# Kernel tuning notes

Measured on AMD Instinct MI355X. Metric: run time of the kernel, lower is better.

## Reference

```python
import jax, jax.numpy as jnp
import numpy as np

ITERS = 2
EPS = 1e-6

_OFFSETS = [(a, b, c) for a in (-1, 0, 1) for b in (-1, 0, 1) for c in (-1, 0, 1)]


def _erosion_step(im):
    # product over full 3x3x3 neighborhood (connectivity=26 -> all 27 voxels),
    # out-of-bounds padded with 1 (identity for product)
    B, C, D, H, W = im.shape
    p = jnp.pad(im, ((0, 0), (0, 0), (1, 1), (1, 1), (1, 1)), constant_values=1.0)
    prod = jnp.ones_like(im)
    for dz, dy, dx in _OFFSETS:
        prod = prod * p[:, :, 1 + dz:1 + dz + D, 1 + dy:1 + dy + H, 1 + dx:1 + dx + W]
    return prod


def _distance_map(im, iters=ITERS):
    # PositiveDistanceMap: dils = -SoftErosion3D(1-im) where SoftErosion3D
    # returns temp = -sum_k im_k (im_0 = 1-im, im_{k+1} = im_k * erosion(im_k))
    cur = 1.0 - im
    acc = jnp.zeros_like(cur)
    for _ in range(iters):
        acc = acc + cur
        cur = cur * _erosion_step(cur)
    return acc


def _lah_loss(x, y_onehot):
    axes = (2, 3, 4)  # batch_lah=False -> per (batch, class) reduction
    dm_hat = _distance_map(x)
    dm_gt = _distance_map(y_onehot)
    fp = (dm_gt * x).sum(axes)
    fn = (dm_hat * y_onehot).sum(axes)
    # norm == 0
    fp = fp / (x.sum(axes) + EPS)
    fn = fn / (y_onehot.sum(axes) + EPS)
    lah = (fp + fn + jnp.abs(fp - fn)) / 2  # logsum2 == elementwise max
    return lah[:, 1:].mean()  # do_bg=False drops background channel


def setup_inputs() -> dict:
    key = jax.random.key(0)
    k1, k2 = jax.random.split(key)
    x = jax.random.uniform(k1, (2, 4, 128, 128, 128), dtype=jnp.float32)
    y = jax.random.randint(k2, (2, 1, 128, 128, 128), 0, 4, dtype=jnp.int64)
    return {"x": x, "y": y}


def reference(x, y):
    C = x.shape[1]
    y_onehot = jax.nn.one_hot(y[:, 0], C, axis=1, dtype=x.dtype)  # [B,C,D,H,W]
    return _lah_loss(x, y_onehot)
```

## Files before the change

### kernel.cpp

```cpp
#include <hip/hip_runtime.h>

constexpr int SPB = 1 << 21;
constexpr float EPSV = 1e-6f;

__device__ unsigned char g_mask[2 * SPB];

constexpr int K0_ZSEG = 4;
constexpr int K0_NBLK = (2 * (128 / K0_ZSEG) * 128) / 4;

struct MEnt { int pk, cx, cy; };

__device__ __forceinline__ MEnt k0_load(const int* __restrict__ yb, int s,
                                        int rbase0, bool ym1, bool yp1) {
    MEnt e;
    const int rb = (s << 14) | rbase0;
    int2 vc = *(const int2*)(yb + rb);
    int nib0 = 1 << vc.x, nib1 = 1 << vc.y;
    if (ym1) { int2 vm = *(const int2*)(yb + rb - 128); nib0 |= 1 << vm.x; nib1 |= 1 << vm.y; }
    if (yp1) { int2 vp = *(const int2*)(yb + rb + 128); nib0 |= 1 << vp.x; nib1 |= 1 << vp.y; }
    e.pk = nib0 | (nib1 << 8);
    e.cx = vc.x; e.cy = vc.y;
    return e;
}

__global__ __launch_bounds__(256) void mask_build(const int* __restrict__ y32) {
    const int wid = (blockIdx.x << 2) | (threadIdx.x >> 6);
    const int lane = threadIdx.x & 63;
    const int yy = wid & 127;
    const int zs = (wid >> 7) & 31;
    const int b = (wid >> 12) & 1;
    const int x0 = lane << 1;
    const int z0 = zs * K0_ZSEG;
    const bool ym1 = yy > 0, yp1 = yy < 127;
    const int rbase0 = (yy << 7) | x0;

    const int* __restrict__ yb = y32 + ((long)b << 21);
    unsigned char* __restrict__ mb = g_mask + ((long)b << 21);

    MEnt e0, e1;
    if (z0 > 0) e0 = k0_load(yb, z0 - 1, rbase0, ym1, yp1);
    else { e0.pk = 0; e0.cx = 0; e0.cy = 0; }
    e1 = k0_load(yb, z0, rbase0, ym1, yp1);

#pragma unroll
    for (int dz = 0; dz < K0_ZSEG; ++dz) {
        const int z = z0 + dz;
        MEnt e2;
        if (z + 1 < 128) e2 = k0_load(yb, z + 1, rbase0, ym1, yp1);
        else { e2.pk = 0; e2.cx = 0; e2.cy = 0; }

        const int zor = e0.pk | e1.pk | e2.pk;
        int orL = __shfl_up(zor, 1);
        if (lane == 0) orL = 0;
        int orR = __shfl_down(zor, 1);
        if (lane == 63) orR = 0;
        const int full0 = (zor | (zor >> 8) | (orL >> 8)) & 15;
        const int full1 = (zor | (zor >> 8) | orR) & 15;

        const unsigned short st =
            (unsigned short)((full0 | (e1.cx << 4)) | ((full1 | (e1.cy << 4)) << 8));
        *(unsigned short*)(mb + ((z << 14) | rbase0)) = st;

        e0 = e1; e1 = e2;
    }
}

constexpr int ZC = 8;
constexpr int NBLK = 8 * 16 * (128 / ZC);

__global__ __launch_bounds__(256) void lah_main(const float* __restrict__ x,
                                                float* __restrict__ acc) {
    __shared__ float raw[4][10][128];
    __shared__ float sred[4];

    const int bid = blockIdx.x;
    const int plane = bid & 7;
    const int b = plane >> 2, cls = plane & 3;
    const int inner = bid >> 3;
    const int yc = inner & 15;
    const int zq = inner >> 4;
    const int r0 = yc * 8;
    const int z0 = zq * ZC;
    const int t = threadIdx.x;
    const int rr = t >> 5;
    const int xc = (t & 31) << 2;
    const int lane = t & 63;
    const int xrow = 8 + (t >> 5);

    const float* __restrict__ xp = x + ((long)plane << 21);
    const unsigned char* __restrict__ mb = g_mask + ((long)b << 21);
    const int mrow = (r0 + rr) << 7;

    const float4 Z4 = make_float4(0.f, 0.f, 0.f, 0.f);

    auto gload = [&](int k, int i) -> float4 {
        const int gr = r0 - 1 + i;
        if ((unsigned)k > 127u || (unsigned)gr > 127u)
            return make_float4(0.f, 0.f, 0.f, 0.f);
        return *(const float4*)(xp + ((k << 14) | (gr << 7) | xc));
    };
    auto stage_direct = [&](int k) {
        const int s = k & 3;
        *(float4*)&raw[s][rr][xc] = gload(k, rr);
        if (t < 64) *(float4*)&raw[s][xrow][xc] = gload(k, xrow);
    };
    auto yprod = [&](int s, float4& cx) -> float4 {
        const float4 a = *(const float4*)&raw[s][rr][xc];
        const float4 bq = *(const float4*)&raw[s][rr + 1][xc];
        const float4 c = *(const float4*)&raw[s][rr + 2][xc];
        cx = bq;
        float4 o;
        o.x = (1.f - a.x) * (1.f - bq.x) * (1.f - c.x);
        o.y = (1.f - a.y) * (1.f - bq.y) * (1.f - c.y);
        o.z = (1.f - a.z) * (1.f - bq.z) * (1.f - c.z);
        o.w = (1.f - a.w) * (1.f - bq.w) * (1.f - c.w);
        return o;
    };

    stage_direct(z0 - 1);
    stage_direct(z0);
    stage_direct(z0 + 1);
    float4 pA = gload(z0 + 2, rr);
    float4 pB = (t < 64) ? gload(z0 + 2, xrow) : Z4;
    __syncthreads();
    float4 cxd, cx0;
    float4 ypm1 = yprod((z0 - 1) & 3, cxd);
    float4 yp0 = yprod(z0 & 3, cx0);
    unsigned mcur = *(const unsigned*)(mb + ((z0 << 14) | mrow | xc));

    float fp = 0.f, fn = 0.f, sx = 0.f, sy = 0.f;

#pragma unroll
    for (int dz = 0; dz < ZC; ++dz) {
        const int z = z0 + dz;

        float4 nA = Z4, nB = Z4;
        if (dz <= ZC - 3) {
            nA = gload(z + 3, rr);
            if (t < 64) nB = gload(z + 3, xrow);
        }
        unsigned mnext = 0;
        if (dz <= ZC - 2)
            mnext = *(const unsigned*)(mb + (((z + 1) << 14) | mrow | xc));

        float4 cx1;
        const float4 ypp1 = yprod((z + 1) & 3, cx1);

        {
            const float zp0 = ypm1.x * yp0.x * ypp1.x;
            const float zp1 = ypm1.y * yp0.y * ypp1.y;
            const float zp2 = ypm1.z * yp0.z * ypp1.z;
            const float zp3 = ypm1.w * yp0.w * ypp1.w;
            float zl = __shfl_up(zp3, 1);
            if ((t & 31) == 0) zl = 1.f;
            float zr = __shfl_down(zp0, 1);
            if ((t & 31) == 31) zr = 1.f;
            const float t01 = zp0 * zp1, t12 = zp1 * zp2, t23 = zp2 * zp3;
            const float P[4] = {zl * t01, t01 * zp2, t12 * zp3, t23 * zr};
            const float xa[4] = {cx0.x, cx0.y, cx0.z, cx0.w};
#pragma unroll
            for (int j = 0; j < 4; ++j) {
                const int m = (mcur >> (j * 8)) & 0xFF;
                const bool pres = (m >> cls) & 1;
                const bool eq = (m >> 4) == cls;
                const float xv = xa[j];
                sx += xv;
                fp += eq ? 0.f : xv * (pres ? 1.f : 2.f);
                fn += eq ? (1.f - xv) * (1.f + P[j]) : 0.f;
                sy += eq ? 1.f : 0.f;
            }
        }

        if (dz <= ZC - 2) {
            const int s = (z + 2) & 3;
            *(float4*)&raw[s][rr][xc] = pA;
            if (t < 64) *(float4*)&raw[s][xrow][xc] = pB;
        }
        __syncthreads();

        pA = nA; pB = nB;
        ypm1 = yp0; yp0 = ypp1; cx0 = cx1; mcur = mnext;
    }

    float rr4[4] = {fp, fn, sx, sy};
#pragma unroll
    for (int i = 0; i < 4; ++i) {
        float vv = rr4[i];
#pragma unroll
        for (int off = 32; off >= 1; off >>= 1) vv += __shfl_down(vv, off);
        rr4[i] = vv;
    }
    if (t < 4) sred[t] = 0.f;
    __syncthreads();
    if (lane == 0) {
#pragma unroll
        for (int i = 0; i < 4; ++i) atomicAdd(&sred[i], rr4[i]);
    }
    __syncthreads();
    if (t < 4)
        atomicAdd(&acc[b * 16 + t * 4 + cls], sred[t]);
}

__global__ void lah_finalize(const float* __restrict__ acc, float* __restrict__ out) {
    float loss = 0.f;
#pragma unroll
    for (int b = 0; b < 2; ++b) {
#pragma unroll
        for (int c = 1; c < 4; ++c) {
            const float fp = acc[b * 16 + 0 + c];
            const float fn = acc[b * 16 + 4 + c];
            const float sxv = acc[b * 16 + 8 + c];
            const float syv = acc[b * 16 + 12 + c];
            loss += fmaxf(fp / (sxv + EPSV), fn / (syv + EPSV));
        }
    }
    out[0] = loss / 6.f;
}

extern "C" void kernel_launch(void* const* d_in, const int* in_sizes, int n_in,
                              void* d_out, int out_size, void* d_ws, size_t ws_size,
                              hipStream_t stream) {
    const float* x = (const float*)d_in[0];
    const int* y32 = (const int*)d_in[1];
    float* out = (float*)d_out;
    float* acc = (float*)d_ws;

    hipMemsetAsync(d_ws, 0, 32 * sizeof(float), stream);
    mask_build<<<K0_NBLK, 256, 0, stream>>>(y32);
    lah_main<<<NBLK, 256, 0, stream>>>(x, acc);
    lah_finalize<<<1, 1, 0, stream>>>(acc, out);
}
```

Baseline: 49.22 us.

## Give each wavefront a private LDS ring to drop per-slice block barriers

Each 64-lane wavefront now owns a two-output-row tile and stages its own four y-rows per z-slice into a wave-private LDS ring. Since no other wave reads that data, the per-iteration __syncthreads is removed, and loads are prefetched two slices ahead. The cost is more halo traffic: each wave loads 4 rows to produce 2, where before 10 rows were loaded to produce 8. It also depends on lockstep execution within a wavefront for the LDS ordering, and the loop unroll changes from full to 4.

```diff
diff --git a/kernel.cpp b/kernel.cpp
--- a/kernel.cpp
+++ b/kernel.cpp
@@ -70,44 +70,56 @@
 
 __global__ __launch_bounds__(256) void lah_main(const float* __restrict__ x,
                                                 float* __restrict__ acc) {
-    __shared__ float raw[4][10][128];
+    __shared__ float lds[4][4][4][128];
     __shared__ float sred[4];
 
     const int bid = blockIdx.x;
     const int plane = bid & 7;
     const int b = plane >> 2, cls = plane & 3;
     const int inner = bid >> 3;
-    const int yc = inner & 15;
+    const int quad = inner & 15;
     const int zq = inner >> 4;
-    const int r0 = yc * 8;
+    const int t = threadIdx.x;
+    const int w = t >> 6;
+    const int rp = quad * 4 + w;
+    const int lane = t & 63;
+    const int half = lane >> 5;
+    const int lx = lane & 31;
+    const int xc = lx << 2;
     const int z0 = zq * ZC;
-    const int t = threadIdx.x;
-    const int rr = t >> 5;
-    const int xc = (t & 31) << 2;
-    const int lane = t & 63;
-    const int xrow = 8 + (t >> 5);
+
+    const int rowA = 2 * rp - 1 + half;
+    const int rowB = 2 * rp + 1 + half;
+    const int rout = 2 * rp + half;
+    const bool okA = rowA >= 0;
+    const bool okB = rowB <= 127;
 
     const float* __restrict__ xp = x + ((long)plane << 21);
     const unsigned char* __restrict__ mb = g_mask + ((long)b << 21);
-    const int mrow = (r0 + rr) << 7;
 
     const float4 Z4 = make_float4(0.f, 0.f, 0.f, 0.f);
 
-    auto gload = [&](int k, int i) -> float4 {
-        const int gr = r0 - 1 + i;
-        if ((unsigned)k > 127u || (unsigned)gr > 127u)
-            return make_float4(0.f, 0.f, 0.f, 0.f);
-        return *(const float4*)(xp + ((k << 14) | (gr << 7) | xc));
-    };
-    auto stage_direct = [&](int k) {
+    auto gloadA = [&](int k) -> float4 {
+        if ((unsigned)k > 127u || !okA) return Z4;
+        return *(const float4*)(xp + ((k << 14) | (rowA << 7) | xc));
+    };
+    auto gloadB = [&](int k) -> float4 {
+        if ((unsigned)k > 127u || !okB) return Z4;
+        return *(const float4*)(xp + ((k << 14) | (rowB << 7) | xc));
+    };
+    auto lmask = [&](int k) -> unsigned {
+        return *(const unsigned*)(mb + ((k << 14) | (rout << 7) | xc));
+    };
+    auto wslice = [&](int k, float4 a, float4 bb) {
         const int s = k & 3;
-        *(float4*)&raw[s][rr][xc] = gload(k, rr);
-        if (t < 64) *(float4*)&raw[s][xrow][xc] = gload(k, xrow);
-    };
-    auto yprod = [&](int s, float4& cx) -> float4 {
-        const float4 a = *(const float4*)&raw[s][rr][xc];
-        const float4 bq = *(const float4*)&raw[s][rr + 1][xc];
-        const float4 c = *(const float4*)&raw[s][rr + 2][xc];
+        *(float4*)&lds[w][s][half][xc] = a;
+        *(float4*)&lds[w][s][2 + half][xc] = bb;
+    };
+    auto yprod = [&](int k, float4& cx) -> float4 {
+        const int s = k & 3;
+        const float4 a = *(const float4*)&lds[w][s][half][xc];
+        const float4 bq = *(const float4*)&lds[w][s][half + 1][xc];
+        const float4 c = *(const float4*)&lds[w][s][half + 2][xc];
         cx = bq;
         float4 o;
         o.x = (1.f - a.x) * (1.f - bq.x) * (1.f - c.x);
@@ -117,34 +129,34 @@
         return o;
     };
 
-    stage_direct(z0 - 1);
-    stage_direct(z0);
-    stage_direct(z0 + 1);
-    float4 pA = gload(z0 + 2, rr);
-    float4 pB = (t < 64) ? gload(z0 + 2, xrow) : Z4;
-    __syncthreads();
+    {
+        float4 a0 = gloadA(z0 - 1), b0 = gloadB(z0 - 1);
+        float4 a1 = gloadA(z0),     b1 = gloadB(z0);
+        wslice(z0 - 1, a0, b0);
+        wslice(z0, a1, b1);
+    }
+    float4 p0A = gloadA(z0 + 1), p0B = gloadB(z0 + 1);
+    float4 p1A = gloadA(z0 + 2), p1B = gloadB(z0 + 2);
+    unsigned mcur = lmask(z0);
     float4 cxd, cx0;
-    float4 ypm1 = yprod((z0 - 1) & 3, cxd);
-    float4 yp0 = yprod(z0 & 3, cx0);
-    unsigned mcur = *(const unsigned*)(mb + ((z0 << 14) | mrow | xc));
+    float4 ypm1 = yprod(z0 - 1, cxd);
+    float4 yp0 = yprod(z0, cx0);
 
     float fp = 0.f, fn = 0.f, sx = 0.f, sy = 0.f;
 
-#pragma unroll
+#pragma unroll 4
     for (int dz = 0; dz < ZC; ++dz) {
         const int z = z0 + dz;
 
         float4 nA = Z4, nB = Z4;
-        if (dz <= ZC - 3) {
-            nA = gload(z + 3, rr);
-            if (t < 64) nB = gload(z + 3, xrow);
-        }
-        unsigned mnext = 0;
-        if (dz <= ZC - 2)
-            mnext = *(const unsigned*)(mb + (((z + 1) << 14) | mrow | xc));
+        if (dz <= ZC - 3) { nA = gloadA(z + 3); nB = gloadB(z + 3); }
+        unsigned mnx = 0;
+        if (dz <= ZC - 2) mnx = lmask(z + 1);
+
+        wslice(z + 1, p0A, p0B);
 
         float4 cx1;
-        const float4 ypp1 = yprod((z + 1) & 3, cx1);
+        const float4 ypp1 = yprod(z + 1, cx1);
 
         {
             const float zp0 = ypm1.x * yp0.x * ypp1.x;
@@ -152,9 +164,9 @@
             const float zp2 = ypm1.z * yp0.z * ypp1.z;
             const float zp3 = ypm1.w * yp0.w * ypp1.w;
             float zl = __shfl_up(zp3, 1);
-            if ((t & 31) == 0) zl = 1.f;
+            if (lx == 0) zl = 1.f;
             float zr = __shfl_down(zp0, 1);
-            if ((t & 31) == 31) zr = 1.f;
+            if (lx == 31) zr = 1.f;
             const float t01 = zp0 * zp1, t12 = zp1 * zp2, t23 = zp2 * zp3;
             const float P[4] = {zl * t01, t01 * zp2, t12 * zp3, t23 * zr};
             const float xa[4] = {cx0.x, cx0.y, cx0.z, cx0.w};
@@ -171,15 +183,8 @@
             }
         }
 
-        if (dz <= ZC - 2) {
-            const int s = (z + 2) & 3;
-            *(float4*)&raw[s][rr][xc] = pA;
-            if (t < 64) *(float4*)&raw[s][xrow][xc] = pB;
-        }
-        __syncthreads();
-
-        pA = nA; pB = nB;
-        ypm1 = yp0; yp0 = ypp1; cx0 = cx1; mcur = mnext;
+        p0A = p1A; p0B = p1B; p1A = nA; p1B = nB;
+        ypm1 = yp0; yp0 = ypp1; cx0 = cx1; mcur = mnx;
     }
 
     float rr4[4] = {fp, fn, sx, sy};
```

Result: slower. 53.01 us (+7.7%).
